# Optimization experiments

Hardware: AMD Instinct MI355X
Metric: run time of the kernel (lower is better)

The kernel has to match this reference:

```python
import jax, jax.numpy as jnp
import numpy as np
from jax import lax

DIM = 192
NUM_HEADS = 4
HEAD_DIM = DIM // NUM_HEADS
EPS_NORM = 1e-12  # F.normalize default eps
EPS_TEMP = 1e-06


def setup_inputs() -> dict:
    key = jax.random.key(0)
    k1, k2, k3, k4 = jax.random.split(key, 4)
    b, c, h, w = 2, DIM, 192, 192
    x = jax.random.normal(k1, (b, c, h, w), dtype=jnp.float32)
    # conv weights, fan-in scaled for sane magnitudes
    w_qkv = jax.random.normal(k2, (3 * DIM, DIM), dtype=jnp.float32) / np.sqrt(DIM)
    w_dw = jax.random.normal(k3, (3 * DIM, 1, 3, 3), dtype=jnp.float32) / 3.0
    w_proj = jax.random.normal(k4, (DIM, DIM), dtype=jnp.float32) / np.sqrt(DIM)
    log_temperature = jnp.zeros((NUM_HEADS, 1, 1), dtype=jnp.float32)
    return {"x": x, "w_qkv": w_qkv, "w_dw": w_dw, "w_proj": w_proj,
            "log_temperature": log_temperature}


def _l2norm_lastdim(t):
    n = jnp.sqrt(jnp.sum(t * t, axis=-1, keepdims=True))
    return t / jnp.maximum(n, EPS_NORM)


def reference(x, w_qkv, w_dw, w_proj, log_temperature):
    b, c, h, w = x.shape
    hw = h * w
    # 1x1 conv (pointwise GEMM over channels)
    qkv = jnp.einsum('oc,bchw->bohw', w_qkv, x)
    # depthwise 3x3 conv, padding=1
    qkv = lax.conv_general_dilated(
        qkv, w_dw, window_strides=(1, 1), padding='SAME',
        feature_group_count=3 * c,
        dimension_numbers=('NCHW', 'OIHW', 'NCHW'))
    q, k, v = jnp.split(qkv, 3, axis=1)
    # [b, heads, head_dim, hw]
    q = q.reshape(b, NUM_HEADS, HEAD_DIM, hw)
    k = k.reshape(b, NUM_HEADS, HEAD_DIM, hw)
    v = v.reshape(b, NUM_HEADS, HEAD_DIM, hw)
    q = _l2norm_lastdim(q)
    k = _l2norm_lastdim(k)
    # channel-wise attention: [b, heads, head_dim, head_dim]
    attn = jnp.einsum('bhdn,bhen->bhde', q, k)
    temperature = jax.nn.softplus(log_temperature) + EPS_TEMP  # [heads,1,1]
    attn = attn * temperature[None]
    attn = jax.nn.softmax(attn, axis=-1)
    out = jnp.einsum('bhde,bhen->bhdn', attn, v)
    out = out.reshape(b, c, h, w)
    return jnp.einsum('oc,bchw->bohw', w_proj, out)
```

## Files before the change

kernel.cpp:

```cpp
#include <hip/hip_runtime.h>
#include <math.h>

#define HW 36864
#define CC 192

typedef __attribute__((ext_vector_type(4))) float f32x4;
typedef __attribute__((ext_vector_type(8))) short bf16x8;

__device__ __forceinline__ float bf2f(unsigned short u) {
    return __uint_as_float(((unsigned int)u) << 16);
}
__device__ __forceinline__ unsigned short f2bf(float f) {
    unsigned int u = __float_as_uint(f);
    unsigned int r = (u + 0x7fffu + ((u >> 16) & 1u)) >> 16;
    return (unsigned short)r;
}

template<bool XF32, bool OUTBF, int NT, int NZ>
__global__ __launch_bounds__(256, 3) void gemm_rpa(
    const unsigned short* __restrict__ A,
    const void* __restrict__ Xv,
    void* __restrict__ Outv,
    long aBatchStride, long xBatchStride, long oBatchStride)
{
    const int nx = gridDim.x;
    int bx = blockIdx.x;
    if ((nx & 7) == 0) {
        const int cpx = nx >> 3;
        bx = (bx & 7) * cpx + (bx >> 3);
    }
    const int z  = (NZ > 1) ? (bx % NZ) : 0;
    const int ng = (NZ > 1) ? (bx / NZ) : bx;
    const int b  = blockIdx.y;
    const int mbase = z * 192;
    const int n00 = ng * (NT * 64);

    const int tid = threadIdx.x;
    const int lane = tid & 63;
    const int wave = tid >> 6;
    const int ml = lane & 15, qk = lane >> 4;
    const int kp = tid & 31;
    const int nc = tid >> 5;

    __shared__ __attribute__((aligned(16))) unsigned short Xs[64 * 202];

    const unsigned short* Ab = A + (long)b * aBatchStride;
    bf16x8 afr[3][6];
#pragma unroll
    for (int f = 0; f < 3; ++f) {
        const unsigned short* row = Ab + (long)(mbase + wave * 48 + f * 16 + ml) * 192 + qk * 8;
#pragma unroll
        for (int kk = 0; kk < 6; ++kk)
            afr[f][kk] = *(const bf16x8*)(row + kk * 32);
    }

    for (int t = 0; t < NT; ++t) {
        const int n0 = n00 + t * 64;

        for (int k0 = 0; k0 < 192; k0 += 64) {
            const int k = k0 + 2 * kp;
            unsigned int pk[8];
            if (XF32) {
                const float* xp = (const float*)Xv + (long)b * xBatchStride + (long)k * HW + n0 + nc * 8;
                float4 a0 = *(const float4*)(xp);
                float4 a1 = *(const float4*)(xp + 4);
                float4 b0 = *(const float4*)(xp + HW);
                float4 b1 = *(const float4*)(xp + HW + 4);
                float lo[8] = {a0.x, a0.y, a0.z, a0.w, a1.x, a1.y, a1.z, a1.w};
                float hi[8] = {b0.x, b0.y, b0.z, b0.w, b1.x, b1.y, b1.z, b1.w};
#pragma unroll
                for (int j = 0; j < 8; ++j)
                    pk[j] = (unsigned int)f2bf(lo[j]) | ((unsigned int)f2bf(hi[j]) << 16);
            } else {
                const unsigned short* xp = (const unsigned short*)Xv + (long)b * xBatchStride + (long)k * HW + n0 + nc * 8;
                int4 r0 = *(const int4*)(xp);
                int4 r1 = *(const int4*)(xp + HW);
                const unsigned short* u0 = (const unsigned short*)&r0;
                const unsigned short* u1 = (const unsigned short*)&r1;
#pragma unroll
                for (int j = 0; j < 8; ++j)
                    pk[j] = (unsigned int)u0[j] | ((unsigned int)u1[j] << 16);
            }
#pragma unroll
            for (int j = 0; j < 8; ++j)
                *(unsigned int*)&Xs[(nc * 8 + j) * 202 + k] = pk[j];
        }
        __syncthreads();

        f32x4 acc[3][4];
#pragma unroll
        for (int f = 0; f < 3; ++f)
#pragma unroll
            for (int s = 0; s < 4; ++s)
                acc[f][s] = (f32x4){0.f, 0.f, 0.f, 0.f};

#pragma unroll
        for (int s = 0; s < 4; ++s) {
#pragma unroll
            for (int kk = 0; kk < 6; ++kk) {
                bf16x8 bfr;
                {
                    const unsigned short* p = &Xs[(s * 16 + ml) * 202 + kk * 32 + qk * 8];
                    union { bf16x8 v; unsigned int u[4]; } tmp;
                    tmp.u[0] = *(const unsigned int*)(p + 0);
                    tmp.u[1] = *(const unsigned int*)(p + 2);
                    tmp.u[2] = *(const unsigned int*)(p + 4);
                    tmp.u[3] = *(const unsigned int*)(p + 6);
                    bfr = tmp.v;
                }
#pragma unroll
                for (int f = 0; f < 3; ++f)
                    acc[f][s] = __builtin_amdgcn_mfma_f32_16x16x32_bf16(afr[f][kk], bfr, acc[f][s], 0, 0, 0);
            }
        }

#pragma unroll
        for (int f = 0; f < 3; ++f) {
            if (OUTBF) {
                unsigned short* Out = (unsigned short*)Outv + (long)b * oBatchStride;
#pragma unroll
                for (int s = 0; s < 4; ++s) {
                    const int gm = mbase + wave * 48 + f * 16 + qk * 4;
                    const int gn = n0 + s * 16 + ml;
#pragma unroll
                    for (int i = 0; i < 4; ++i)
                        Out[(long)(gm + i) * HW + gn] = f2bf(acc[f][s][i]);
                }
            } else {
                float* Out = (float*)Outv + (long)b * oBatchStride;
#pragma unroll
                for (int s = 0; s < 4; ++s) {
                    const int gm = mbase + wave * 48 + f * 16 + qk * 4;
                    const int gn = n0 + s * 16 + ml;
#pragma unroll
                    for (int i = 0; i < 4; ++i)
                        Out[(long)(gm + i) * HW + gn] = acc[f][s][i];
                }
            }
        }

        if (t + 1 < NT) __syncthreads();
    }
}

__global__ __launch_bounds__(256) void dwconv_kernel(
    const unsigned short* __restrict__ qkv,
    const float* __restrict__ wdw,
    unsigned short* __restrict__ dwout,
    float* __restrict__ ssq)
{
    const int ht = blockIdx.x;
    const int ch = blockIdx.y;
    const int b  = blockIdx.z;
    const int tid = threadIdx.x;
    const int lane = tid & 63;
    const int h0 = ht * 8;
    const int t  = tid & 31;
    const int hh = tid >> 5;
    const bool active = (t < 24);

    const float* wp = wdw + ch * 9;
    const float w00 = wp[0], w01 = wp[1], w02 = wp[2];
    const float w10 = wp[3], w11 = wp[4], w12 = wp[5];
    const float w20 = wp[6], w21 = wp[7], w22 = wp[8];

    const long chbase = (long)(b * 576 + ch) * HW;

    float x[3][8];
#pragma unroll
    for (int dy = 0; dy < 3; ++dy) {
        const int hr = h0 + hh + dy - 1;
        int4 ld = make_int4(0, 0, 0, 0);
        if (active && hr >= 0 && hr < 192)
            ld = *(const int4*)(qkv + chbase + (long)hr * 192 + t * 8);
        const unsigned short* u = (const unsigned short*)&ld;
#pragma unroll
        for (int j = 0; j < 8; ++j) x[dy][j] = bf2f(u[j]);
    }

    float lft[3], rgt[3];
#pragma unroll
    for (int dy = 0; dy < 3; ++dy) {
        float l = __shfl(x[dy][7], lane - 1, 64);
        float r = __shfl(x[dy][0], lane + 1, 64);
        lft[dy] = (t == 0) ? 0.f : l;
        rgt[dy] = (t >= 23) ? 0.f : r;
    }

    float acc[8];
#pragma unroll
    for (int j = 0; j < 8; ++j) {
        float a0 = (j == 0) ? lft[0] : x[0][j - 1];
        float a2 = (j == 7) ? rgt[0] : x[0][j + 1];
        float b0 = (j == 0) ? lft[1] : x[1][j - 1];
        float b2 = (j == 7) ? rgt[1] : x[1][j + 1];
        float c0 = (j == 0) ? lft[2] : x[2][j - 1];
        float c2 = (j == 7) ? rgt[2] : x[2][j + 1];
        acc[j] = w00 * a0 + w01 * x[0][j] + w02 * a2
               + w10 * b0 + w11 * x[1][j] + w12 * b2
               + w20 * c0 + w21 * x[2][j] + w22 * c2;
    }

    if (active) {
        int4 st;
        unsigned short* u = (unsigned short*)&st;
#pragma unroll
        for (int j = 0; j < 8; ++j) u[j] = f2bf(acc[j]);
        *(int4*)(dwout + chbase + (long)(h0 + hh) * 192 + t * 8) = st;
    }

    if (ch < 384) {
        float mysq = 0.f;
        if (active) {
#pragma unroll
            for (int j = 0; j < 8; ++j) mysq += acc[j] * acc[j];
        }
#pragma unroll
        for (int off = 32; off > 0; off >>= 1) mysq += __shfl_xor(mysq, off, 64);
        __shared__ float red[4];
        if (lane == 0) red[tid >> 6] = mysq;
        __syncthreads();
        if (tid == 0) atomicAdd(&ssq[b * 384 + ch], red[0] + red[1] + red[2] + red[3]);
    }
}

__global__ __launch_bounds__(256) void gram_kernel(
    const unsigned short* __restrict__ dwb, float* __restrict__ gram)
{
    const int chunk = blockIdx.x;
    const int bh = blockIdx.y;
    const int b = bh >> 2, h = bh & 3;
    const int tid = threadIdx.x;
    const int wave = tid >> 6;
    const int lane = tid & 63;
    const int row = lane & 15, qk = lane >> 4;
    const long n0 = (long)chunk * 512 + wave * 128;

    const unsigned short* qb = dwb + (long)(b * 576 + h * 48) * HW + n0;
    const unsigned short* kb = dwb + (long)(b * 576 + 192 + h * 48) * HW + n0;

    f32x4 acc[3][3];
#pragma unroll
    for (int f = 0; f < 3; ++f)
#pragma unroll
        for (int g = 0; g < 3; ++g) acc[f][g] = (f32x4){0.f, 0.f, 0.f, 0.f};

#pragma unroll
    for (int kk = 0; kk < 128; kk += 32) {
        const int col = kk + qk * 8;
        bf16x8 aq[3], bk[3];
#pragma unroll
        for (int f = 0; f < 3; ++f) aq[f] = *(const bf16x8*)(qb + (long)(f * 16 + row) * HW + col);
#pragma unroll
        for (int g = 0; g < 3; ++g) bk[g] = *(const bf16x8*)(kb + (long)(g * 16 + row) * HW + col);
#pragma unroll
        for (int f = 0; f < 3; ++f)
#pragma unroll
            for (int g = 0; g < 3; ++g)
                acc[f][g] = __builtin_amdgcn_mfma_f32_16x16x32_bf16(aq[f], bk[g], acc[f][g], 0, 0, 0);
    }

    __shared__ float sg[4][64][37];
#pragma unroll
    for (int f = 0; f < 3; ++f)
#pragma unroll
        for (int g = 0; g < 3; ++g)
#pragma unroll
            for (int i = 0; i < 4; ++i)
                sg[wave][lane][f * 12 + g * 4 + i] = acc[f][g][i];
    __syncthreads();

    const int rl = tid >> 2;
    const int i0 = (tid & 3) * 9;
    const int rrow = rl & 15, rqk = rl >> 4;
    float* gb = gram + bh * 2304;
#pragma unroll
    for (int j = 0; j < 9; ++j) {
        const int idx = i0 + j;
        const float v = sg[0][rl][idx] + sg[1][rl][idx] + sg[2][rl][idx] + sg[3][rl][idx];
        const int f = idx / 12, rem = idx - f * 12, g = rem >> 2, i = rem & 3;
        atomicAdd(&gb[(f * 16 + rqk * 4 + i) * 48 + g * 16 + rrow], v);
    }
}

__global__ __launch_bounds__(64) void attn_kernel(
    const float* __restrict__ gram, const float* __restrict__ ssq,
    const float* __restrict__ lt, float* __restrict__ attn)
{
    const int bh = blockIdx.x;
    const int b = bh >> 2, h = bh & 3;
    const int d = threadIdx.x;
    if (d >= 48) return;
    const float temp = log1pf(expf(lt[h])) + 1e-6f;
    const float invq = 1.f / fmaxf(sqrtf(ssq[b * 384 + h * 48 + d]), 1e-12f);
    float p[48];
    float mx = -1e30f;
#pragma unroll
    for (int e = 0; e < 48; ++e) {
        float invk = 1.f / fmaxf(sqrtf(ssq[b * 384 + 192 + h * 48 + e]), 1e-12f);
        float g = gram[bh * 2304 + d * 48 + e] * invq * invk * temp;
        p[e] = g;
        mx = fmaxf(mx, g);
    }
    float sum = 0.f;
#pragma unroll
    for (int e = 0; e < 48; ++e) { float x = expf(p[e] - mx); p[e] = x; sum += x; }
    const float inv = 1.f / sum;
#pragma unroll
    for (int e = 0; e < 48; ++e) attn[bh * 2304 + d * 48 + e] = p[e] * inv;
}

__global__ __launch_bounds__(192) void mproj_kernel(
    const float* __restrict__ wproj, const float* __restrict__ attn,
    unsigned short* __restrict__ Mb)
{
    const int o = blockIdx.x;
    const int b = blockIdx.y;
    const int he = threadIdx.x;
    const int h = he / 48, e = he - h * 48;
    const float* ar = attn + ((b * 4 + h) * 48) * 48 + e;
    const float* wr = wproj + o * 192 + h * 48;
    float acc = 0.f;
#pragma unroll
    for (int d = 0; d < 48; ++d) acc += wr[d] * ar[d * 48];
    Mb[(long)(b * 192 + o) * 192 + he] = f2bf(acc);
}

__global__ void cvt_bf16_kernel(const float* __restrict__ in,
                                unsigned short* __restrict__ out, int n)
{
    int i = blockIdx.x * 256 + threadIdx.x;
    if (i < n) out[i] = f2bf(in[i]);
}

extern "C" void kernel_launch(void* const* d_in, const int* in_sizes, int n_in,
                              void* d_out, int out_size, void* d_ws, size_t ws_size,
                              hipStream_t stream)
{
    const float* x      = (const float*)d_in[0];
    const float* w_qkv  = (const float*)d_in[1];
    const float* w_dw   = (const float*)d_in[2];
    const float* w_proj = (const float*)d_in[3];
    const float* lt     = (const float*)d_in[4];

    char* ws = (char*)d_ws;
    unsigned short* wqkv_b = (unsigned short*)(ws + 0);
    float* gram            = (float*)(ws + 221184);
    float* ssq             = (float*)(ws + 294912);
    float* attn            = (float*)(ws + 297984);
    unsigned short* Mb     = (unsigned short*)(ws + 371712);
    unsigned short* qkvb   = (unsigned short*)(ws + 524288);
    unsigned short* dwb    = (unsigned short*)(ws + 524288 + 84934656ll);

    hipMemsetAsync(gram, 0, 73728 + 3072, stream);

    cvt_bf16_kernel<<<dim3((110592 + 255) / 256), 256, 0, stream>>>(w_qkv, wqkv_b, 110592);

    gemm_rpa<true, true, 3, 3><<<dim3(576, 2), 256, 0, stream>>>(
        wqkv_b, (const void*)x, (void*)qkvb,
        0L, (long)192 * HW, (long)576 * HW);

    dwconv_kernel<<<dim3(24, 576, 2), 256, 0, stream>>>(qkvb, w_dw, dwb, ssq);

    gram_kernel<<<dim3(72, 8), 256, 0, stream>>>(dwb, gram);

    attn_kernel<<<dim3(8), 64, 0, stream>>>(gram, ssq, lt, attn);

    mproj_kernel<<<dim3(192, 2), 192, 0, stream>>>(w_proj, attn, Mb);

    gemm_rpa<false, false, 2, 1><<<dim3(288, 2), 256, 0, stream>>>(
        Mb, (const void*)(dwb + (long)384 * HW), d_out,
        (long)192 * 192, (long)576 * HW, (long)192 * HW);
}
```

Measured before the change: 267.8 us.

## Software-pipeline GEMM X loads and pre-convert x to bf16

The GEMM now streams the X operand in 64-wide k-sections, with the global load for stage g+2 issued before the compute of stage g and the shared-memory write for g+1 done afterwards. Global latency is meant to overlap with MFMA work instead of being exposed each tile. The first GEMM no longer converts fp32 x inline; a separate kernel converts x to bf16 into the dwconv output buffer first. This adds a full extra read/write pass over x and one more barrier per k-section, in exchange for halving the GEMM's input traffic.

```diff
diff --git a/kernel.cpp b/kernel.cpp
--- a/kernel.cpp
+++ b/kernel.cpp
@@ -16,10 +16,10 @@
     return (unsigned short)r;
 }
 
-template<bool XF32, bool OUTBF, int NT, int NZ>
+template<bool OUTBF, int NT, int NZ>
 __global__ __launch_bounds__(256, 3) void gemm_rpa(
     const unsigned short* __restrict__ A,
-    const void* __restrict__ Xv,
+    const unsigned short* __restrict__ X,
     void* __restrict__ Outv,
     long aBatchStride, long xBatchStride, long oBatchStride)
 {
@@ -54,53 +54,40 @@
             afr[f][kk] = *(const bf16x8*)(row + kk * 32);
     }
 
-    for (int t = 0; t < NT; ++t) {
-        const int n0 = n00 + t * 64;
-
-        for (int k0 = 0; k0 < 192; k0 += 64) {
-            const int k = k0 + 2 * kp;
-            unsigned int pk[8];
-            if (XF32) {
-                const float* xp = (const float*)Xv + (long)b * xBatchStride + (long)k * HW + n0 + nc * 8;
-                float4 a0 = *(const float4*)(xp);
-                float4 a1 = *(const float4*)(xp + 4);
-                float4 b0 = *(const float4*)(xp + HW);
-                float4 b1 = *(const float4*)(xp + HW + 4);
-                float lo[8] = {a0.x, a0.y, a0.z, a0.w, a1.x, a1.y, a1.z, a1.w};
-                float hi[8] = {b0.x, b0.y, b0.z, b0.w, b1.x, b1.y, b1.z, b1.w};
-#pragma unroll
-                for (int j = 0; j < 8; ++j)
-                    pk[j] = (unsigned int)f2bf(lo[j]) | ((unsigned int)f2bf(hi[j]) << 16);
-            } else {
-                const unsigned short* xp = (const unsigned short*)Xv + (long)b * xBatchStride + (long)k * HW + n0 + nc * 8;
-                int4 r0 = *(const int4*)(xp);
-                int4 r1 = *(const int4*)(xp + HW);
-                const unsigned short* u0 = (const unsigned short*)&r0;
-                const unsigned short* u1 = (const unsigned short*)&r1;
-#pragma unroll
-                for (int j = 0; j < 8; ++j)
-                    pk[j] = (unsigned int)u0[j] | ((unsigned int)u1[j] << 16);
-            }
-#pragma unroll
-            for (int j = 0; j < 8; ++j)
-                *(unsigned int*)&Xs[(nc * 8 + j) * 202 + k] = pk[j];
-        }
-        __syncthreads();
-
-        f32x4 acc[3][4];
-#pragma unroll
-        for (int f = 0; f < 3; ++f)
-#pragma unroll
-            for (int s = 0; s < 4; ++s)
-                acc[f][s] = (f32x4){0.f, 0.f, 0.f, 0.f};
-
+    const unsigned short* Xg = X + (long)b * xBatchStride + n00 + nc * 8;
+
+    f32x4 acc[3][4];
+#pragma unroll
+    for (int f = 0; f < 3; ++f)
+#pragma unroll
+        for (int s = 0; s < 4; ++s)
+            acc[f][s] = (f32x4){0.f, 0.f, 0.f, 0.f};
+
+    auto LOAD = [&](int g, int4* r) {
+        const int t = g / 3, sec = g - 3 * t;
+        const unsigned short* p = Xg + (long)(sec * 64 + 2 * kp) * HW + t * 64;
+        r[0] = *(const int4*)(p);
+        r[1] = *(const int4*)(p + HW);
+    };
+    auto WRITE = [&](int g, const int4* r) {
+        const int t = g / 3, sec = g - 3 * t;
+        const int k = sec * 64 + 2 * kp;
+        const unsigned short* u0 = (const unsigned short*)&r[0];
+        const unsigned short* u1 = (const unsigned short*)&r[1];
+#pragma unroll
+        for (int j = 0; j < 8; ++j)
+            *(unsigned int*)&Xs[(nc * 8 + j) * 202 + k] =
+                (unsigned int)u0[j] | ((unsigned int)u1[j] << 16);
+    };
+    auto COMPUTE = [&](int g) {
+        const int sec = g % 3;
 #pragma unroll
         for (int s = 0; s < 4; ++s) {
 #pragma unroll
-            for (int kk = 0; kk < 6; ++kk) {
+            for (int kl = 0; kl < 2; ++kl) {
                 bf16x8 bfr;
                 {
-                    const unsigned short* p = &Xs[(s * 16 + ml) * 202 + kk * 32 + qk * 8];
+                    const unsigned short* p = &Xs[(s * 16 + ml) * 202 + sec * 64 + kl * 32 + qk * 8];
                     union { bf16x8 v; unsigned int u[4]; } tmp;
                     tmp.u[0] = *(const unsigned int*)(p + 0);
                     tmp.u[1] = *(const unsigned int*)(p + 2);
@@ -110,36 +97,51 @@
                 }
 #pragma unroll
                 for (int f = 0; f < 3; ++f)
-                    acc[f][s] = __builtin_amdgcn_mfma_f32_16x16x32_bf16(afr[f][kk], bfr, acc[f][s], 0, 0, 0);
+                    acc[f][s] = __builtin_amdgcn_mfma_f32_16x16x32_bf16(afr[f][sec * 2 + kl], bfr, acc[f][s], 0, 0, 0);
             }
         }
-
+    };
+    auto STORE = [&](int t) {
+        const int n0 = n00 + t * 64;
 #pragma unroll
         for (int f = 0; f < 3; ++f) {
-            if (OUTBF) {
-                unsigned short* Out = (unsigned short*)Outv + (long)b * oBatchStride;
-#pragma unroll
-                for (int s = 0; s < 4; ++s) {
-                    const int gm = mbase + wave * 48 + f * 16 + qk * 4;
-                    const int gn = n0 + s * 16 + ml;
-#pragma unroll
-                    for (int i = 0; i < 4; ++i)
-                        Out[(long)(gm + i) * HW + gn] = f2bf(acc[f][s][i]);
+#pragma unroll
+            for (int s = 0; s < 4; ++s) {
+                const int gm = mbase + wave * 48 + f * 16 + qk * 4;
+                const int gn = n0 + s * 16 + ml;
+#pragma unroll
+                for (int i = 0; i < 4; ++i) {
+                    if (OUTBF)
+                        ((unsigned short*)Outv)[(long)b * oBatchStride + (long)(gm + i) * HW + gn] = f2bf(acc[f][s][i]);
+                    else
+                        ((float*)Outv)[(long)b * oBatchStride + (long)(gm + i) * HW + gn] = acc[f][s][i];
                 }
-            } else {
-                float* Out = (float*)Outv + (long)b * oBatchStride;
-#pragma unroll
-                for (int s = 0; s < 4; ++s) {
-                    const int gm = mbase + wave * 48 + f * 16 + qk * 4;
-                    const int gn = n0 + s * 16 + ml;
-#pragma unroll
-                    for (int i = 0; i < 4; ++i)
-                        Out[(long)(gm + i) * HW + gn] = acc[f][s][i];
-                }
+                acc[f][s] = (f32x4){0.f, 0.f, 0.f, 0.f};
             }
         }
-
-        if (t + 1 < NT) __syncthreads();
+    };
+
+    constexpr int NS = NT * 3;
+    int4 sA[2], sB[2];
+
+    LOAD(0, sA);
+    WRITE(0, sA);
+    LOAD(1, sB);
+    __syncthreads();
+
+#pragma unroll
+    for (int g = 0; g < NS; ++g) {
+        if ((g & 1) == 0) {
+            if (g + 2 < NS) LOAD(g + 2, sA);
+            COMPUTE(g);
+            if (g + 1 < NS) WRITE(g + 1, sB);
+        } else {
+            if (g + 2 < NS) LOAD(g + 2, sB);
+            COMPUTE(g);
+            if (g + 1 < NS) WRITE(g + 1, sA);
+        }
+        if (g % 3 == 2) STORE(g / 3);
+        if (g + 1 < NS) __syncthreads();
     }
 }
 
@@ -333,6 +335,19 @@
     if (i < n) out[i] = f2bf(in[i]);
 }
 
+__global__ __launch_bounds__(256) void cvt_x_kernel(
+    const float* __restrict__ in, unsigned short* __restrict__ out)
+{
+    const long i = ((long)blockIdx.x * 256 + threadIdx.x) * 8;
+    float4 a = *(const float4*)(in + i);
+    float4 b = *(const float4*)(in + i + 4);
+    int4 st;
+    unsigned short* u = (unsigned short*)&st;
+    u[0] = f2bf(a.x); u[1] = f2bf(a.y); u[2] = f2bf(a.z); u[3] = f2bf(a.w);
+    u[4] = f2bf(b.x); u[5] = f2bf(b.y); u[6] = f2bf(b.z); u[7] = f2bf(b.w);
+    *(int4*)(out + i) = st;
+}
+
 extern "C" void kernel_launch(void* const* d_in, const int* in_sizes, int n_in,
                               void* d_out, int out_size, void* d_ws, size_t ws_size,
                               hipStream_t stream)
@@ -351,13 +366,16 @@
     unsigned short* Mb     = (unsigned short*)(ws + 371712);
     unsigned short* qkvb   = (unsigned short*)(ws + 524288);
     unsigned short* dwb    = (unsigned short*)(ws + 524288 + 84934656ll);
+    unsigned short* xbf    = dwb;
 
     hipMemsetAsync(gram, 0, 73728 + 3072, stream);
 
     cvt_bf16_kernel<<<dim3((110592 + 255) / 256), 256, 0, stream>>>(w_qkv, wqkv_b, 110592);
 
-    gemm_rpa<true, true, 3, 3><<<dim3(576, 2), 256, 0, stream>>>(
-        wqkv_b, (const void*)x, (void*)qkvb,
+    cvt_x_kernel<<<dim3(6912), 256, 0, stream>>>(x, xbf);
+
+    gemm_rpa<true, 3, 3><<<dim3(576, 2), 256, 0, stream>>>(
+        wqkv_b, xbf, (void*)qkvb,
         0L, (long)192 * HW, (long)576 * HW);
 
     dwconv_kernel<<<dim3(24, 576, 2), 256, 0, stream>>>(qkvb, w_dw, dwb, ssq);
@@ -368,7 +386,7 @@
 
     mproj_kernel<<<dim3(192, 2), 192, 0, stream>>>(w_proj, attn, Mb);
 
-    gemm_rpa<false, false, 2, 1><<<dim3(288, 2), 256, 0, stream>>>(
-        Mb, (const void*)(dwb + (long)384 * HW), d_out,
+    gemm_rpa<false, 2, 1><<<dim3(288, 2), 256, 0, stream>>>(
+        Mb, dwb + (long)384 * HW, d_out,
         (long)192 * 192, (long)576 * HW, (long)192 * HW);
 }
```

Result: no change. 266.6 us (-0.4%).
